# Kernel optimization log

Measured on AMD Instinct MI355X. Metric: run time of the kernel, lower is better.

Reference implementation:

```python
import jax, jax.numpy as jnp
import numpy as np

BN_EPS = 1e-5


def conv1x1(x, w, b):
    # x: [B,C,H,W] (NCHW), w: [Cout,Cin], b: [Cout]
    return jnp.einsum('bchw,oc->bohw', x, w) + b[None, :, None, None]


def dw_bn(x, w_dw, b_dw, scale, bias, mean, var):
    # depthwise 1x1 conv (per-channel affine) followed by eval-mode BatchNorm
    z = x * w_dw[None, :, None, None] + b_dw[None, :, None, None]
    inv = scale / jnp.sqrt(var + BN_EPS)
    return (z - mean[None, :, None, None]) * inv[None, :, None, None] + bias[None, :, None, None]


def setup_inputs() -> dict:
    B, C, W, H = 16, 728, 38, 38
    key = jax.random.key(0)
    ks = jax.random.split(key, 24)
    s = 1.0 / np.sqrt(C)
    d = {
        'x_FAD': jax.random.normal(ks[0], (B, C, W, H), jnp.float32),
        'x_LFS': jax.random.normal(ks[1], (B, C, W, H), jnp.float32),
        'Wq_fad': jax.random.normal(ks[2], (C, C), jnp.float32) * s,
        'bq_fad': jax.random.normal(ks[3], (C,), jnp.float32) * s,
        'Wq_lfs': jax.random.normal(ks[4], (C, C), jnp.float32) * s,
        'bq_lfs': jax.random.normal(ks[5], (C,), jnp.float32) * s,
        'Wk_fad': jax.random.normal(ks[6], (C, C), jnp.float32) * s,
        'bk_fad': jax.random.normal(ks[7], (C,), jnp.float32) * s,
        'Wk_lfs': jax.random.normal(ks[8], (C, C), jnp.float32) * s,
        'bk_lfs': jax.random.normal(ks[9], (C,), jnp.float32) * s,
        'gamma_fad': jnp.zeros((1,), jnp.float32),
        'gamma_lfs': jnp.zeros((1,), jnp.float32),
        'dw_fad_w': jax.random.normal(ks[10], (C,), jnp.float32),
        'dw_fad_b': jax.random.normal(ks[11], (C,), jnp.float32) * 0.1,
        'dw_lfs_w': jax.random.normal(ks[12], (C,), jnp.float32),
        'dw_lfs_b': jax.random.normal(ks[13], (C,), jnp.float32) * 0.1,
        'fad_bn_scale': jnp.ones((C,), jnp.float32) + 0.1 * jax.random.normal(ks[14], (C,), jnp.float32),
        'fad_bn_bias': 0.1 * jax.random.normal(ks[15], (C,), jnp.float32),
        'fad_bn_mean': 0.1 * jax.random.normal(ks[16], (C,), jnp.float32),
        'fad_bn_var': jnp.abs(jax.random.normal(ks[17], (C,), jnp.float32)) + 0.5,
        'lfs_bn_scale': jnp.ones((C,), jnp.float32) + 0.1 * jax.random.normal(ks[18], (C,), jnp.float32),
        'lfs_bn_bias': 0.1 * jax.random.normal(ks[19], (C,), jnp.float32),
        'lfs_bn_mean': 0.1 * jax.random.normal(ks[20], (C,), jnp.float32),
        'lfs_bn_var': jnp.abs(jax.random.normal(ks[21], (C,), jnp.float32)) + 0.5,
    }
    return d


def reference(x_FAD, x_LFS, Wq_fad, bq_fad, Wq_lfs, bq_lfs, Wk_fad, bk_fad, Wk_lfs, bk_lfs,
              gamma_fad, gamma_lfs, dw_fad_w, dw_fad_b, dw_lfs_w, dw_lfs_b,
              fad_bn_scale, fad_bn_bias, fad_bn_mean, fad_bn_var,
              lfs_bn_scale, lfs_bn_bias, lfs_bn_mean, lfs_bn_var):
    B, C, W, H = x_FAD.shape  # W == H
    q_FAD = conv1x1(x_FAD, Wq_fad, bq_fad).reshape(B * C, W, H)
    q_LFS = conv1x1(x_LFS, Wq_lfs, bq_lfs).reshape(B * C, W, H)
    M_query = jnp.concatenate([q_FAD, q_LFS], axis=2)              # [BC, W, 2H]
    k_FAD = conv1x1(x_FAD, Wk_fad, bk_fad).reshape(B * C, W, H).transpose(0, 2, 1)
    k_LFS = conv1x1(x_LFS, Wk_lfs, bk_lfs).reshape(B * C, W, H).transpose(0, 2, 1)
    M_key = jnp.concatenate([k_FAD, k_LFS], axis=1)                # [BC, 2H, W]
    energy = jnp.einsum('bij,bjk->bik', M_query, M_key)            # [BC, W, W]
    attention = jax.nn.softmax(energy, axis=-1).reshape(B, C, W, W)
    g_lfs = jax.nn.sigmoid(gamma_lfs) * 2.0 - 1.0                  # scalar (shape [1])
    g_fad = jax.nn.sigmoid(gamma_fad) * 2.0 - 1.0
    att_LFS = x_LFS * attention * g_lfs
    y_FAD = x_FAD + dw_bn(att_LFS, dw_fad_w, dw_fad_b, fad_bn_scale, fad_bn_bias, fad_bn_mean, fad_bn_var)
    att_FAD = x_FAD * attention * g_fad
    y_LFS = x_LFS + dw_bn(att_FAD, dw_lfs_w, dw_lfs_b, lfs_bn_scale, lfs_bn_bias, lfs_bn_mean, lfs_bn_var)
    return (y_FAD, y_LFS)
```

## Files before the change

kernel.cpp:

```cpp
#include <hip/hip_runtime.h>

typedef unsigned short u16;
typedef __bf16 bf16x8 __attribute__((ext_vector_type(8)));
typedef u16 u16x8 __attribute__((ext_vector_type(8)));
typedef float floatx4 __attribute__((ext_vector_type(4)));

#define NB 16
#define NC 728
#define HW 38
#define NP 1444
#define NPIX 16819712
#define K2 736
#define P2 1536
#define M2 768

__device__ __forceinline__ u16 f2bf(float f) {
  union { float f; unsigned int i; } v; v.f = f;
  unsigned int r = v.i + 0x7FFFu + ((v.i >> 16) & 1u);
  return (u16)(r >> 16);
}

__device__ __forceinline__ void async16(const u16* g, u16* l) {
  __builtin_amdgcn_global_load_lds((__attribute__((address_space(1))) void*)g,
                                   (__attribute__((address_space(3))) void*)l,
                                   16, 0, 0);
}

__global__ void prep_params(const float* __restrict__ gF, const float* __restrict__ gL,
                            const float* __restrict__ dwfw, const float* __restrict__ dwfb,
                            const float* __restrict__ dwlw, const float* __restrict__ dwlb,
                            const float* __restrict__ fs, const float* __restrict__ fb,
                            const float* __restrict__ fm, const float* __restrict__ fv,
                            const float* __restrict__ ls, const float* __restrict__ lb,
                            const float* __restrict__ lm, const float* __restrict__ lv,
                            float* __restrict__ mulF, float* __restrict__ addF,
                            float* __restrict__ mulL, float* __restrict__ addL) {
  int c = blockIdx.x * 256 + threadIdx.x;
  if (c >= NC) return;
  float gf = 2.f / (1.f + __expf(-gF[0])) - 1.f;
  float gl = 2.f / (1.f + __expf(-gL[0])) - 1.f;
  float invf = fs[c] * rsqrtf(fv[c] + 1e-5f);
  mulF[c] = gl * dwfw[c] * invf;
  addF[c] = (dwfb[c] - fm[c]) * invf + fb[c];
  float invl = ls[c] * rsqrtf(lv[c] + 1e-5f);
  mulL[c] = gf * dwlw[c] * invl;
  addL[c] = (dwlb[c] - lm[c]) * invl + lb[c];
}

__global__ __launch_bounds__(256) void transpose_pad(const float* __restrict__ xF,
                                                     const float* __restrict__ xL,
                                                     u16* __restrict__ xTF,
                                                     u16* __restrict__ xTL,
                                                     int bbase, int ng) {
  __shared__ u16 tile[64][68];
  int z = blockIdx.z;
  int tensor = (z >= ng) ? 1 : 0;
  int bl = z - (tensor ? ng : 0);
  int b = bbase + bl;
  const float* x = tensor ? xL : xF;
  u16* xT = tensor ? xTL : xTF;
  int p0 = blockIdx.x * 64, c0 = blockIdx.y * 64;
  int t = threadIdx.x;
  int pl4 = (t & 15) * 4, csub = t >> 4;
  bool fullp = (p0 + 63) < NP;
#pragma unroll
  for (int it = 0; it < 4; ++it) {
    int cl = it * 16 + csub;
    int c = c0 + cl, p = p0 + pl4;
    u16 o0v = 0, o1 = 0, o2 = 0, o3 = 0;
    if (c < NC) {
      const float* src = &x[(size_t)(b * NC + c) * NP + p];
      if (fullp) {
        float4 v = *(const float4*)src;
        o0v = f2bf(v.x); o1 = f2bf(v.y); o2 = f2bf(v.z); o3 = f2bf(v.w);
      } else {
        if (p + 0 < NP) o0v = f2bf(src[0]);
        if (p + 1 < NP) o1 = f2bf(src[1]);
        if (p + 2 < NP) o2 = f2bf(src[2]);
        if (p + 3 < NP) o3 = f2bf(src[3]);
      }
    }
    tile[cl][pl4] = o0v; tile[cl][pl4 + 1] = o1; tile[cl][pl4 + 2] = o2; tile[cl][pl4 + 3] = o3;
  }
  __syncthreads();
  int cl2 = t & 31, psub = t >> 5;
#pragma unroll
  for (int it = 0; it < 8; ++it) {
    int pl = psub * 8 + it;
    int c = c0 + cl2 * 2;
    if (c < K2) {
      unsigned int v = (unsigned int)tile[cl2 * 2][pl] | (((unsigned int)tile[cl2 * 2 + 1][pl]) << 16);
      *(unsigned int*)&xT[(size_t)(bl * P2 + p0 + pl) * K2 + c] = v;
    }
  }
}

__global__ void pad_weights(const float* __restrict__ W0, const float* __restrict__ W1,
                            const float* __restrict__ W2, const float* __restrict__ W3,
                            u16* __restrict__ Wpad) {
  int combo = blockIdx.y;
  const float* W = combo == 0 ? W0 : combo == 1 ? W1 : combo == 2 ? W2 : W3;
  int idx = blockIdx.x * 256 + threadIdx.x;
  if (idx >= M2 * K2) return;
  int r = idx / K2, c = idx - r * K2;
  u16 v = (r < NC && c < NC) ? f2bf(W[r * NC + c]) : (u16)0;
  Wpad[(size_t)combo * (M2 * K2) + idx] = v;
}

__global__ __launch_bounds__(256) void conv_gemm(const u16* __restrict__ Wpad,
                                                 const u16* __restrict__ xTF,
                                                 const u16* __restrict__ xTL,
                                                 const float* __restrict__ b0, const float* __restrict__ b1,
                                                 const float* __restrict__ b2, const float* __restrict__ b3,
                                                 u16* __restrict__ Qf, u16* __restrict__ Kf,
                                                 u16* __restrict__ Ql, u16* __restrict__ Kl) {
  __shared__ __align__(16) u16 A_lds[2][128 * 32];
  __shared__ __align__(16) u16 B_lds[2][128 * 32];
  int t = threadIdx.x;
  int lane = t & 63, w = t >> 6;

  unsigned int f = blockIdx.x + 12u * (blockIdx.y + 12u * blockIdx.z);
  unsigned int nwg = 144u * gridDim.z;
  unsigned int q = nwg >> 3;
  unsigned int wid = (f & 7u) * q + (f >> 3);
  unsigned int xc = wid % 12u;
  unsigned int r1 = wid / 12u;
  unsigned int pt = r1 % 12u;
  unsigned int zz = r1 / 12u;
  int bl = (int)(zz >> 1);
  int th = (int)(zz & 1u);
  int combo = th * 2 + (xc >= 6u ? 1 : 0);
  int o0 = (int)(xc % 6u) * 128;
  int p0 = (int)pt * 128;

  const u16* Wb = Wpad + (size_t)combo * (M2 * K2);
  const u16* Xb = (th == 0 ? xTF : xTL) + (size_t)bl * (P2 * K2);
  const float* bias = combo == 0 ? b0 : combo == 1 ? b1 : combo == 2 ? b2 : b3;
  u16* Out = combo == 0 ? Qf : combo == 1 ? Kf : combo == 2 ? Ql : Kl;

  const u16* Ag = Wb + (size_t)(o0 + w * 32 + (lane >> 2)) * K2 + (lane & 3) * 8;
  const u16* Bg = Xb + (size_t)(p0 + w * 32 + (lane >> 2)) * K2 + (lane & 3) * 8;

  floatx4 acc[4][4] = {};
  int wm = w >> 1, wn = w & 1;
  int ln = lane & 15, qd = lane >> 4;
  int rdoff = (wm * 64 + ln) * 32 + qd * 8;
  int rdoffB = (wn * 64 + ln) * 32 + qd * 8;

  {
    u16* Al = &A_lds[0][w * 32 * 32];
    u16* Bl = &B_lds[0][w * 32 * 32];
    async16(Ag, Al);
    async16(Ag + 16 * K2, Al + 16 * 32);
    async16(Bg, Bl);
    async16(Bg + 16 * K2, Bl + 16 * 32);
  }
  __syncthreads();

  int cur = 0;
  for (int kt = 0; kt < 23; ++kt) {
    if (kt + 1 < 23) {
      int ko = (kt + 1) * 32;
      u16* Al = &A_lds[cur ^ 1][w * 32 * 32];
      u16* Bl = &B_lds[cur ^ 1][w * 32 * 32];
      async16(Ag + ko, Al);
      async16(Ag + ko + 16 * K2, Al + 16 * 32);
      async16(Bg + ko, Bl);
      async16(Bg + ko + 16 * K2, Bl + 16 * 32);
    }
    const u16* Ard = &A_lds[cur][rdoff];
    const u16* Brd = &B_lds[cur][rdoffB];
    bf16x8 af[4], bfv[4];
#pragma unroll
    for (int mt = 0; mt < 4; ++mt) af[mt] = *(const bf16x8*)(Ard + mt * 16 * 32);
#pragma unroll
    for (int nt = 0; nt < 4; ++nt) bfv[nt] = *(const bf16x8*)(Brd + nt * 16 * 32);
#pragma unroll
    for (int mt = 0; mt < 4; ++mt)
#pragma unroll
      for (int nt = 0; nt < 4; ++nt)
        acc[mt][nt] = __builtin_amdgcn_mfma_f32_16x16x32_bf16(af[mt], bfv[nt], acc[mt][nt], 0, 0, 0);
    __syncthreads();
    cur ^= 1;
  }

#pragma unroll
  for (int mt = 0; mt < 4; ++mt)
#pragma unroll
    for (int reg = 0; reg < 4; ++reg) {
      int o_r = o0 + wm * 64 + mt * 16 + qd * 4 + reg;
      if (o_r < NC) {
        float bv = bias[o_r];
#pragma unroll
        for (int nt = 0; nt < 4; ++nt) {
          int p_c = p0 + wn * 64 + nt * 16 + ln;
          if (p_c < NP) Out[(size_t)(bl * NC + o_r) * NP + p_c] = f2bf(acc[mt][nt][reg] + bv);
        }
      }
    }
}

__global__ __launch_bounds__(64) void attn_final(const u16* __restrict__ Qf, const u16* __restrict__ Kf,
                                                 const u16* __restrict__ Ql, const u16* __restrict__ Kl,
                                                 const float* __restrict__ xF, const float* __restrict__ xL,
                                                 const float* __restrict__ mulF, const float* __restrict__ addF,
                                                 const float* __restrict__ mulL, const float* __restrict__ addL,
                                                 float* __restrict__ out, int bbase) {
  __shared__ __align__(16) u16 q_lds[48 * 96];
  __shared__ __align__(16) u16 k_lds[48 * 96];
  int bc = blockIdx.x;
  int bl = bc / NC, c = bc - bl * NC;
  int t = threadIdx.x;
  int base = bc * NP;
  int gbase = ((bbase + bl) * NC + c) * NP;

  for (int i = t; i < 38 * 5; i += 64) {
    int r = i / 5, c2 = (i - r * 5) * 2;
    *(unsigned int*)&q_lds[r * 96 + 38 + c2] = 0;
    *(unsigned int*)&q_lds[r * 96 + 86 + c2] = 0;
    *(unsigned int*)&k_lds[r * 96 + 38 + c2] = 0;
    *(unsigned int*)&k_lds[r * 96 + 86 + c2] = 0;
  }

#define STAGE(SRC, DST, COL0)                                              \
  {                                                                        \
    _Pragma("unroll") for (int s = 0; s < 3; ++s) {                        \
      int e0 = (s * 64 + t) * 8;                                           \
      if (e0 < NP) {                                                       \
        u16x8 v = *(const u16x8*)(SRC + base + e0);                        \
        int r = e0 / 38, cc = e0 - r * 38;                                 \
        _Pragma("unroll") for (int j = 0; j < 8; ++j) {                    \
          if (e0 + j < NP) DST[r * 96 + (COL0) + cc] = v[j];               \
          if (++cc == 38) { cc = 0; ++r; }                                 \
        }                                                                  \
      }                                                                    \
    }                                                                      \
  }
  STAGE(Qf, q_lds, 0)
  STAGE(Ql, q_lds, 48)
  STAGE(Kf, k_lds, 0)
  STAGE(Kl, k_lds, 48)
#undef STAGE
  __syncthreads();

  int ln = t & 15, qd = t >> 4;
  floatx4 acc[3][3] = {};
#pragma unroll
  for (int ks = 0; ks < 3; ++ks) {
    bf16x8 af[3], bfv[3];
#pragma unroll
    for (int mt = 0; mt < 3; ++mt) af[mt] = *(const bf16x8*)&q_lds[(mt * 16 + ln) * 96 + ks * 32 + qd * 8];
#pragma unroll
    for (int nt = 0; nt < 3; ++nt) bfv[nt] = *(const bf16x8*)&k_lds[(nt * 16 + ln) * 96 + ks * 32 + qd * 8];
#pragma unroll
    for (int mt = 0; mt < 3; ++mt)
#pragma unroll
      for (int nt = 0; nt < 3; ++nt)
        acc[mt][nt] = __builtin_amdgcn_mfma_f32_16x16x32_bf16(af[mt], bfv[nt], acc[mt][nt], 0, 0, 0);
  }
  float rinv[3][4];
#pragma unroll
  for (int mt = 0; mt < 3; ++mt)
#pragma unroll
    for (int reg = 0; reg < 4; ++reg) {
      float m = -1e30f;
#pragma unroll
      for (int nt = 0; nt < 3; ++nt)
        if (nt * 16 + ln < HW) m = fmaxf(m, acc[mt][nt][reg]);
#pragma unroll
      for (int off = 8; off > 0; off >>= 1) m = fmaxf(m, __shfl_xor(m, off, 16));
      float s = 0.f;
#pragma unroll
      for (int nt = 0; nt < 3; ++nt) {
        float v = (nt * 16 + ln < HW) ? __expf(acc[mt][nt][reg] - m) : 0.f;
        acc[mt][nt][reg] = v;
        s += v;
      }
#pragma unroll
      for (int off = 8; off > 0; off >>= 1) s += __shfl_xor(s, off, 16);
      rinv[mt][reg] = 1.f / s;
    }

  __syncthreads();
  float* att = (float*)q_lds;
#pragma unroll
  for (int mt = 0; mt < 3; ++mt)
#pragma unroll
    for (int reg = 0; reg < 4; ++reg) {
      int i = mt * 16 + qd * 4 + reg;
      if (i < HW) {
#pragma unroll
        for (int nt = 0; nt < 3; ++nt) {
          int k = nt * 16 + ln;
          if (k < HW) att[i * HW + k] = acc[mt][nt][reg] * rinv[mt][reg];
        }
      }
    }
  __syncthreads();

  float mf = mulF[c], adf = addF[c], ml = mulL[c], adl = addL[c];
#pragma unroll
  for (int s = 0; s < 6; ++s) {
    int p = s * 256 + t * 4;
    if (p < NP) {
      float4 a  = *(const float4*)&att[p];
      float4 xf = *(const float4*)&xF[gbase + p];
      float4 xl = *(const float4*)&xL[gbase + p];
      float4 yf, yl;
      yf.x = fmaf(xl.x * a.x, mf, xf.x + adf); yl.x = fmaf(xf.x * a.x, ml, xl.x + adl);
      yf.y = fmaf(xl.y * a.y, mf, xf.y + adf); yl.y = fmaf(xf.y * a.y, ml, xl.y + adl);
      yf.z = fmaf(xl.z * a.z, mf, xf.z + adf); yl.z = fmaf(xf.z * a.z, ml, xl.z + adl);
      yf.w = fmaf(xl.w * a.w, mf, xf.w + adf); yl.w = fmaf(xf.w * a.w, ml, xl.w + adl);
      *(float4*)&out[gbase + p] = yf;
      *(float4*)&out[NPIX + gbase + p] = yl;
    }
  }
}

extern "C" void kernel_launch(void* const* d_in, const int* in_sizes, int n_in,
                              void* d_out, int out_size, void* d_ws, size_t ws_size,
                              hipStream_t stream) {
  (void)in_sizes; (void)n_in; (void)out_size;
  const float* xF   = (const float*)d_in[0];
  const float* xL   = (const float*)d_in[1];
  const float* Wq_f = (const float*)d_in[2];
  const float* bq_f = (const float*)d_in[3];
  const float* Wq_l = (const float*)d_in[4];
  const float* bq_l = (const float*)d_in[5];
  const float* Wk_f = (const float*)d_in[6];
  const float* bk_f = (const float*)d_in[7];
  const float* Wk_l = (const float*)d_in[8];
  const float* bk_l = (const float*)d_in[9];
  const float* gF   = (const float*)d_in[10];
  const float* gL   = (const float*)d_in[11];
  const float* dwfw = (const float*)d_in[12];
  const float* dwfb = (const float*)d_in[13];
  const float* dwlw = (const float*)d_in[14];
  const float* dwlb = (const float*)d_in[15];
  const float* fs   = (const float*)d_in[16];
  const float* fb   = (const float*)d_in[17];
  const float* fm   = (const float*)d_in[18];
  const float* fv   = (const float*)d_in[19];
  const float* ls   = (const float*)d_in[20];
  const float* lb   = (const float*)d_in[21];
  const float* lm   = (const float*)d_in[22];
  const float* lv   = (const float*)d_in[23];

  const size_t small_bytes = 4 * (size_t)NC * sizeof(float);
  const size_t wpad_bytes  = (size_t)4 * M2 * K2 * 2;
  const size_t perb_bytes  = (size_t)2 * P2 * K2 * 2
                           + (size_t)4 * NC * NP * 2;
  int ng = 16;
  while (ng > 4 && small_bytes + wpad_bytes + (size_t)ng * perb_bytes > ws_size) ng >>= 1;

  char* ws = (char*)d_ws;
  size_t off = 0;
  float* mulF = (float*)(ws + off); off += NC * sizeof(float);
  float* addF = (float*)(ws + off); off += NC * sizeof(float);
  float* mulL = (float*)(ws + off); off += NC * sizeof(float);
  float* addL = (float*)(ws + off); off += NC * sizeof(float);
  off = (off + 15) & ~(size_t)15;
  u16* Wpad = (u16*)(ws + off); off += wpad_bytes;
  u16* xTF  = (u16*)(ws + off); off += (size_t)ng * P2 * K2 * 2;
  u16* xTL  = (u16*)(ws + off); off += (size_t)ng * P2 * K2 * 2;
  u16* Qf   = (u16*)(ws + off); off += (size_t)ng * NC * NP * 2;
  u16* Kf   = (u16*)(ws + off); off += (size_t)ng * NC * NP * 2;
  u16* Ql   = (u16*)(ws + off); off += (size_t)ng * NC * NP * 2;
  u16* Kl   = (u16*)(ws + off); off += (size_t)ng * NC * NP * 2;

  prep_params<<<dim3(3), dim3(256), 0, stream>>>(gF, gL, dwfw, dwfb, dwlw, dwlb,
                                                 fs, fb, fm, fv, ls, lb, lm, lv,
                                                 mulF, addF, mulL, addL);
  pad_weights<<<dim3((M2 * K2 + 255) / 256, 4), dim3(256), 0, stream>>>(Wq_f, Wk_f, Wq_l, Wk_l, Wpad);
  for (int g = 0; g < NB; g += ng) {
    transpose_pad<<<dim3(P2 / 64, 12, 2 * ng), dim3(256), 0, stream>>>(xF, xL, xTF, xTL, g, ng);
    conv_gemm<<<dim3(12, 12, 2 * ng), dim3(256), 0, stream>>>(Wpad, xTF, xTL,
                                                              bq_f, bk_f, bq_l, bk_l,
                                                              Qf, Kf, Ql, Kl);
    attn_final<<<dim3(ng * NC), dim3(64), 0, stream>>>(Qf, Kf, Ql, Kl, xF, xL,
                                                       mulF, addF, mulL, addL,
                                                       (float*)d_out, g);
  }
}
```

Measured before the change: 618.4 us.

## Pre-swizzle weights into MFMA fragment order and load A directly from global

The weight padding kernel now writes bf16 weights in MFMA-fragment order (16-row groups by 32-wide k tiles, 64 lanes by 8 elements), so each lane can load its A fragment with one contiguous 16-byte global read. The conv GEMM drops the A shared-memory double buffer and its async copies, keeping LDS staging only for the activation operand. This cuts LDS traffic and footprint, but A reads now hit global/L2 synchronously inside the k-loop with no prefetch, which can expose latency.

Measured after the change: 615.5 us. No clear change (-0.5%).

```diff
diff --git a/kernel.cpp b/kernel.cpp
--- a/kernel.cpp
+++ b/kernel.cpp
@@ -102,9 +102,14 @@
   const float* W = combo == 0 ? W0 : combo == 1 ? W1 : combo == 2 ? W2 : W3;
   int idx = blockIdx.x * 256 + threadIdx.x;
   if (idx >= M2 * K2) return;
-  int r = idx / K2, c = idx - r * K2;
-  u16 v = (r < NC && c < NC) ? f2bf(W[r * NC + c]) : (u16)0;
-  Wpad[(size_t)combo * (M2 * K2) + idx] = v;
+  int j = idx & 7;
+  int l = (idx >> 3) & 63;
+  int v = idx >> 9;
+  int kt = v % 23, og = v / 23;
+  int row = og * 16 + (l & 15);
+  int col = kt * 32 + (l >> 4) * 8 + j;
+  u16 val = (row < NC && col < NC) ? f2bf(W[row * NC + col]) : (u16)0;
+  Wpad[(size_t)combo * (M2 * K2) + idx] = val;
 }
 
 __global__ __launch_bounds__(256) void conv_gemm(const u16* __restrict__ Wpad,
@@ -114,7 +119,6 @@
                                                  const float* __restrict__ b2, const float* __restrict__ b3,
                                                  u16* __restrict__ Qf, u16* __restrict__ Kf,
                                                  u16* __restrict__ Ql, u16* __restrict__ Kl) {
-  __shared__ __align__(16) u16 A_lds[2][128 * 32];
   __shared__ __align__(16) u16 B_lds[2][128 * 32];
   int t = threadIdx.x;
   int lane = t & 63, w = t >> 6;
@@ -133,48 +137,38 @@
   int o0 = (int)(xc % 6u) * 128;
   int p0 = (int)pt * 128;
 
-  const u16* Wb = Wpad + (size_t)combo * (M2 * K2);
+  const u16* WbS = Wpad + (size_t)combo * (M2 * K2);
   const u16* Xb = (th == 0 ? xTF : xTL) + (size_t)bl * (P2 * K2);
   const float* bias = combo == 0 ? b0 : combo == 1 ? b1 : combo == 2 ? b2 : b3;
   u16* Out = combo == 0 ? Qf : combo == 1 ? Kf : combo == 2 ? Ql : Kl;
 
-  const u16* Ag = Wb + (size_t)(o0 + w * 32 + (lane >> 2)) * K2 + (lane & 3) * 8;
   const u16* Bg = Xb + (size_t)(p0 + w * 32 + (lane >> 2)) * K2 + (lane & 3) * 8;
 
   floatx4 acc[4][4] = {};
   int wm = w >> 1, wn = w & 1;
   int ln = lane & 15, qd = lane >> 4;
-  int rdoff = (wm * 64 + ln) * 32 + qd * 8;
+  const u16* Afrag = WbS + (size_t)((o0 >> 4) + wm * 4) * 23 * 512 + (size_t)lane * 8;
   int rdoffB = (wn * 64 + ln) * 32 + qd * 8;
 
-  {
-    u16* Al = &A_lds[0][w * 32 * 32];
-    u16* Bl = &B_lds[0][w * 32 * 32];
-    async16(Ag, Al);
-    async16(Ag + 16 * K2, Al + 16 * 32);
-    async16(Bg, Bl);
-    async16(Bg + 16 * K2, Bl + 16 * 32);
-  }
+  async16(Bg, &B_lds[0][w * 32 * 32]);
+  async16(Bg + 16 * K2, &B_lds[0][w * 32 * 32 + 16 * 32]);
   __syncthreads();
 
   int cur = 0;
   for (int kt = 0; kt < 23; ++kt) {
     if (kt + 1 < 23) {
       int ko = (kt + 1) * 32;
-      u16* Al = &A_lds[cur ^ 1][w * 32 * 32];
       u16* Bl = &B_lds[cur ^ 1][w * 32 * 32];
-      async16(Ag + ko, Al);
-      async16(Ag + ko + 16 * K2, Al + 16 * 32);
       async16(Bg + ko, Bl);
       async16(Bg + ko + 16 * K2, Bl + 16 * 32);
     }
-    const u16* Ard = &A_lds[cur][rdoff];
-    const u16* Brd = &B_lds[cur][rdoffB];
     bf16x8 af[4], bfv[4];
 #pragma unroll
-    for (int mt = 0; mt < 4; ++mt) af[mt] = *(const bf16x8*)(Ard + mt * 16 * 32);
-#pragma unroll
-    for (int nt = 0; nt < 4; ++nt) bfv[nt] = *(const bf16x8*)(Brd + nt * 16 * 32);
+    for (int mt = 0; mt < 4; ++mt)
+      af[mt] = *(const bf16x8*)(Afrag + (size_t)(mt * 23 + kt) * 512);
+#pragma unroll
+    for (int nt = 0; nt < 4; ++nt)
+      bfv[nt] = *(const bf16x8*)&B_lds[cur][rdoffB + nt * 16 * 32];
 #pragma unroll
     for (int mt = 0; mt < 4; ++mt)
 #pragma unroll
```
